# Kernel optimization log

Hardware: AMD Instinct MI355X
Metric: run time of the kernel (lower is better)

Reference implementation:

```python
import jax, jax.numpy as jnp
import numpy as np

H = 256        # h_dim
H2 = 128       # h_dim // 2
S = 512        # sentence_size
G = 64         # number of component graphs in the batched graph
NN = 100000    # total nodes in batched graph
NE = 200000    # total edges
NENT = 20000   # num entities
NREL = 500     # num relations
B = 32         # batch of query timestamps
SEQ = 10       # seq_len


def setup_inputs() -> dict:
    key = jax.random.key(0)
    ks = jax.random.split(key, 32)
    d = {}
    d["node_ids"] = jax.random.randint(ks[0], (NN,), 0, NENT, dtype=jnp.int32)
    d["edge_src"] = jax.random.randint(ks[1], (NE,), 0, NN, dtype=jnp.int32)
    d["edge_dst"] = jax.random.randint(ks[2], (NE,), 0, NN, dtype=jnp.int32)
    d["edge_type"] = jax.random.randint(ks[3], (NE,), 0, NREL, dtype=jnp.int32)
    d["node2graph"] = jnp.sort(jax.random.randint(ks[4], (NN,), 0, G, dtype=jnp.int32))
    d["edge2graph"] = jnp.sort(jax.random.randint(ks[5], (NE,), 0, G, dtype=jnp.int32))
    d["text_emb"] = jax.random.normal(ks[6], (NE, S), dtype=jnp.float32)
    d["time_idx"] = jax.random.randint(ks[7], (B, SEQ), 0, G, dtype=jnp.int32)
    d["len_non_zero"] = jnp.maximum(jax.random.randint(ks[8], (B,), 0, SEQ, dtype=jnp.int32), 1)
    d["ent_embeds"] = jax.random.normal(ks[9], (NENT, 2 * H), dtype=jnp.float32) * 0.05
    d["ent_memory"] = jax.random.normal(ks[10], (NENT, H), dtype=jnp.float32) * 0.05
    d["rel_embeds"] = jax.random.normal(ks[11], (NREL, 2 * H), dtype=jnp.float32) * 0.05
    d["rel_memory"] = jax.random.normal(ks[12], (NREL, H), dtype=jnp.float32) * 0.05
    sc = lambda k, sh: jax.random.normal(k, sh, dtype=jnp.float32) * (1.0 / np.sqrt(sh[0]))
    d["w_node_W"] = sc(ks[13], (3 * H, H)); d["w_node_b"] = jnp.zeros((H,), jnp.float32)
    d["w_rel_W"] = sc(ks[14], (3 * H, H)); d["w_rel_b"] = jnp.zeros((H,), jnp.float32)
    # CompGCN layer 1: H -> H2 (nodes and edges), text S -> H2
    d["Wn1"] = sc(ks[15], (H, H2)); d["Wl1"] = sc(ks[16], (H, H2))
    d["Wt1"] = sc(ks[17], (S, H2)); d["Wr1"] = sc(ks[18], (H, H2))
    d["b1"] = jnp.zeros((H2,), jnp.float32)
    # CompGCN layer 2: H2 -> H, text S -> H
    d["Wn2"] = sc(ks[19], (H2, H)); d["Wl2"] = sc(ks[20], (H2, H))
    d["Wt2"] = sc(ks[21], (S, H)); d["Wr2"] = sc(ks[22], (H2, H))
    d["b2"] = jnp.zeros((H,), jnp.float32)
    return d


def _compgcn_layer(h, e, text, src, dst, Wn, Wl, Wt, Wr, b, n_nodes):
    # composition = subtraction: msg = (h_src - e_h) @ Wn + text @ Wt
    msg = (h[src] - e) @ Wn + text @ Wt                      # [NE, out]
    agg = jax.ops.segment_sum(msg, dst, num_segments=n_nodes)
    deg = jax.ops.segment_sum(jnp.ones((msg.shape[0],), msg.dtype), dst, num_segments=n_nodes)
    agg = agg / jnp.maximum(deg, 1.0)[:, None]
    h_new = jax.nn.relu(agg + h @ Wl + b)                    # self-loop + bias + relu
    e_new = jax.nn.relu(e @ Wr)                              # relation transform
    return h_new, e_new


def reference(node_ids, edge_src, edge_dst, edge_type, node2graph, edge2graph,
              text_emb, time_idx, len_non_zero,
              ent_embeds, ent_memory, rel_embeds, rel_memory,
              w_node_W, w_node_b, w_rel_W, w_rel_b,
              Wn1, Wl1, Wt1, Wr1, b1, Wn2, Wl2, Wt2, Wr2, b2):
    n_nodes = node_ids.shape[0]
    # initial node / edge features: cat(embed[2h], memory[h]) -> Linear(3h, h)
    h = jnp.concatenate([ent_embeds[node_ids], ent_memory[node_ids]], axis=1) @ w_node_W + w_node_b
    e = jnp.concatenate([rel_embeds[edge_type], rel_memory[edge_type]], axis=1) @ w_rel_W + w_rel_b
    # two CompGCN relational message-passing layers: H -> H2 -> H
    h, e = _compgcn_layer(h, e, text_emb, edge_src, edge_dst, Wn1, Wl1, Wt1, Wr1, b1, n_nodes)
    h, e = _compgcn_layer(h, e, text_emb, edge_src, edge_dst, Wn2, Wl2, Wt2, Wr2, b2, n_nodes)
    # dgl.max_nodes / dgl.max_edges: per-graph max pooling (maxpool == 1)
    gn = jax.ops.segment_max(h, node2graph, num_segments=G)   # [G, H]
    ge = jax.ops.segment_max(e, edge2graph, num_segments=G)   # [G, H]
    global_info = jnp.concatenate([gn, ge], axis=-1)          # [G, 2H]
    # ragged temporal gather: embed_seq[i, j] = global_info[time_to_idx[time_list[i][j]]]
    seq = global_info[time_idx]                               # [B, SEQ, 2H]
    mask = (jnp.arange(SEQ, dtype=jnp.int32)[None, :] < len_non_zero[:, None])
    seq = seq * mask[..., None].astype(seq.dtype)             # zeros past len_non_zero
    # dropout at eval time is identity
    return seq, len_non_zero
```

## Files before the change

### kernel.cpp

```cpp
#include <hip/hip_runtime.h>

#define HD    256
#define HD2   128
#define SDIM  512
#define GNUM  64
#define NN    100000
#define NE    200000
#define NENT  20000
#define NREL  500
#define BNUM  32
#define SEQL  10

typedef __attribute__((ext_vector_type(4))) float f32x4;
typedef __attribute__((ext_vector_type(8))) short bf16x8;

__device__ __forceinline__ short to_bf(float f) {
    unsigned u = __float_as_uint(f);
    u += 0x7fff + ((u >> 16) & 1);
    return (short)(u >> 16);
}
__device__ __forceinline__ float bf_to_f(unsigned short u) {
    return __uint_as_float(((unsigned)u) << 16);
}


__global__ void k_cnt(const int* __restrict__ edst, int* __restrict__ cnt) {
    int e = blockIdx.x * 256 + threadIdx.x;
    if (e < NE) atomicAdd(&cnt[edst[e]], 1);
}

__global__ void k_scan_blk(const int* __restrict__ cnt, int* __restrict__ row_off,
                           int* __restrict__ bsum) {
    __shared__ int s[256];
    int i = blockIdx.x * 256 + threadIdx.x;
    int v = cnt[i];
    s[threadIdx.x] = v;
    __syncthreads();
    for (int d = 1; d < 256; d <<= 1) {
        int t = (threadIdx.x >= d) ? s[threadIdx.x - d] : 0;
        __syncthreads();
        s[threadIdx.x] += t;
        __syncthreads();
    }
    row_off[i] = s[threadIdx.x] - v;
    if (threadIdx.x == 255) bsum[blockIdx.x] = s[255];
}

__global__ void k_scan_top(int* __restrict__ bsum) {
    __shared__ int s[512];
    int v = (threadIdx.x < 391) ? bsum[threadIdx.x] : 0;
    s[threadIdx.x] = v;
    __syncthreads();
    for (int d = 1; d < 512; d <<= 1) {
        int t = (threadIdx.x >= d) ? s[threadIdx.x - d] : 0;
        __syncthreads();
        s[threadIdx.x] += t;
        __syncthreads();
    }
    if (threadIdx.x < 391) bsum[threadIdx.x] = s[threadIdx.x] - v;
}

__global__ void k_scan_add(int* __restrict__ row_off, const int* __restrict__ bsum,
                           int* __restrict__ cur) {
    int i = blockIdx.x * 256 + threadIdx.x;
    int v = row_off[i] + bsum[blockIdx.x];
    row_off[i] = v;
    cur[i] = v;
}

__global__ void k_fill(const int* __restrict__ edst, const int* __restrict__ esrc,
                       const int* __restrict__ etype, const int* __restrict__ node_ids,
                       int* __restrict__ cur, int* __restrict__ pinv,
                       int* __restrict__ esrcC, int* __restrict__ etC,
                       int* __restrict__ nidC) {
    int e = blockIdx.x * 256 + threadIdx.x;
    if (e < NE) {
        int pos = atomicAdd(&cur[edst[e]], 1);
        int s = esrc[e];
        pinv[e] = pos;
        esrcC[pos] = s;
        etC[pos] = etype[e];
        nidC[pos] = node_ids[s];
    }
}


__global__ void k_rel_feat(const float* __restrict__ rel_emb, const float* __restrict__ rel_mem,
                           const float* __restrict__ W, const float* __restrict__ b,
                           float* __restrict__ rel_feat) {
    __shared__ float s[768];
    int r = blockIdx.x, j = threadIdx.x;
    for (int k = j; k < 768; k += 256)
        s[k] = (k < 512) ? rel_emb[r * 512 + k] : rel_mem[r * 256 + (k - 512)];
    __syncthreads();
    float acc = b[j];
    for (int k = 0; k < 768; ++k) acc += s[k] * W[k * 256 + j];
    rel_feat[r * 256 + j] = acc;
}

__global__ void k_rel_l1(const float* __restrict__ rel_feat, const float* __restrict__ Wn1,
                         const float* __restrict__ Wr1, float* __restrict__ ecomb,
                         float* __restrict__ er1) {
    __shared__ float s[256];
    int r = blockIdx.x, j = threadIdx.x;
    s[j] = rel_feat[r * 256 + j];
    __syncthreads();
    if (j < 128) {
        float acc = 0.f;
        for (int k = 0; k < 256; ++k) acc += s[k] * Wn1[k * 128 + j];
        ecomb[r * 384 + j] = acc;
    } else {
        int jj = j - 128;
        float acc = 0.f;
        for (int k = 0; k < 256; ++k) acc += s[k] * Wr1[k * 128 + jj];
        er1[r * 128 + jj] = fmaxf(acc, 0.f);
    }
}

__global__ void k_rel_l2(const float* __restrict__ er1, const float* __restrict__ Wr2,
                         const float* __restrict__ Wn2, float* __restrict__ er2,
                         float* __restrict__ ecomb) {
    __shared__ float s[128];
    int r = blockIdx.x, j = threadIdx.x;
    if (j < 128) s[j] = er1[r * 128 + j];
    __syncthreads();
    float a = 0.f, c = 0.f;
    for (int k = 0; k < 128; ++k) {
        float v = s[k];
        a += v * Wr2[k * 256 + j];
        c += v * Wn2[k * 256 + j];
    }
    er2[r * 256 + j] = fmaxf(a, 0.f);
    ecomb[r * 384 + 128 + j] = c;
}


__global__ void k_cw(const float* __restrict__ wnW, const float* __restrict__ Wn1,
                     const float* __restrict__ Wl1, float* __restrict__ cw) {
    __shared__ float s[256];
    int k = blockIdx.x, j = threadIdx.x;
    s[j] = wnW[k * 256 + j];
    __syncthreads();
    float acc = 0.f;
    if (j < 128) {
        for (int m = 0; m < 256; ++m) acc += s[m] * Wn1[m * 128 + j];
    } else {
        int jj = j - 128;
        for (int m = 0; m < 256; ++m) acc += s[m] * Wl1[m * 128 + jj];
    }
    cw[k * 256 + j] = acc;
}

__global__ void k_cb(const float* __restrict__ wnb, const float* __restrict__ Wn1,
                     const float* __restrict__ Wl1, float* __restrict__ bc) {
    int j = threadIdx.x;
    float acc = 0.f;
    if (j < 128) {
        for (int m = 0; m < 256; ++m) acc += wnb[m] * Wn1[m * 128 + j];
    } else {
        int jj = j - 128;
        for (int m = 0; m < 256; ++m) acc += wnb[m] * Wl1[m * 128 + jj];
    }
    bc[j] = acc;
}

__global__ void k_pack(const float* __restrict__ src, bf16x8* __restrict__ dst,
                       int K, int N) {
    int KF = K >> 5;
    int fid = blockIdx.x;
    int n = fid / KF, kk = fid - n * KF;
    int lane = threadIdx.x;
    int col = n * 16 + (lane & 15);
    int kb = kk * 32 + (lane >> 4) * 8;
    bf16x8 v;
#pragma unroll
    for (int j = 0; j < 8; ++j) v[j] = to_bf(src[(size_t)(kb + j) * N + col]);
    dst[(size_t)fid * 64 + lane] = v;
}


__global__ void __launch_bounds__(256) k_ent(const float* __restrict__ ee,
                                             const float* __restrict__ em,
                                             const bf16x8* __restrict__ cwf,
                                             const float* __restrict__ bc,
                                             float* __restrict__ ha1,
                                             float* __restrict__ hb1) {
    __shared__ bf16x8 sA[2048];
    int tid = threadIdx.x;
    int e0 = blockIdx.x * 64;
    int wave = tid >> 6, lane = tid & 63;
    int gs = (tid >> 4) & 3, rs = tid & 15;
    int rowS = ((tid >> 6) & 3) * 16 + rs;
    int ent = e0 + rowS;
    if (ent >= NENT) ent = NENT - 1;
    f32x4 acc[4][4];
#pragma unroll
    for (int mf = 0; mf < 4; ++mf)
#pragma unroll
        for (int nf = 0; nf < 4; ++nf) acc[mf][nf] = (f32x4)0.f;

    for (int ch = 0; ch < 3; ++ch) {
        if (ch) __syncthreads();
#pragma unroll
        for (int it = 0; it < 8; ++it) {
            int gc = ch * 256 + it * 32 + gs * 8;
            const float4* p = (gc < 512)
                ? (const float4*)(ee + (size_t)ent * 512 + gc)
                : (const float4*)(em + (size_t)ent * 256 + (gc - 512));
            float4 x = p[0], y = p[1];
            bf16x8 v;
            v[0] = to_bf(x.x); v[1] = to_bf(x.y); v[2] = to_bf(x.z); v[3] = to_bf(x.w);
            v[4] = to_bf(y.x); v[5] = to_bf(y.y); v[6] = to_bf(y.z); v[7] = to_bf(y.w);
            sA[it * 256 + tid] = v;
        }
        __syncthreads();
#pragma unroll
        for (int kkl = 0; kkl < 8; ++kkl) {
            bf16x8 a[4], b[4];
#pragma unroll
            for (int mf = 0; mf < 4; ++mf) a[mf] = sA[kkl * 256 + mf * 64 + lane];
#pragma unroll
            for (int nf = 0; nf < 4; ++nf)
                b[nf] = cwf[(size_t)((wave * 4 + nf) * 24 + ch * 8 + kkl) * 64 + lane];
#pragma unroll
            for (int mf = 0; mf < 4; ++mf)
#pragma unroll
                for (int nf = 0; nf < 4; ++nf)
                    acc[mf][nf] = __builtin_amdgcn_mfma_f32_16x16x32_bf16(a[mf], b[nf],
                                                                          acc[mf][nf], 0, 0, 0);
        }
    }
    int gq = lane >> 4, cl = lane & 15;
#pragma unroll
    for (int mf = 0; mf < 4; ++mf)
#pragma unroll
        for (int nf = 0; nf < 4; ++nf) {
            int c = wave * 64 + nf * 16 + cl;
            float bb = bc[c];
#pragma unroll
            for (int q = 0; q < 4; ++q) {
                int m = e0 + mf * 16 + gq * 4 + q;
                if (m < NENT) {
                    float val = acc[mf][nf][q] + bb;
                    if (c < 128) ha1[(size_t)m * 128 + c] = val;
                    else hb1[(size_t)m * 128 + (c - 128)] = val;
                }
            }
        }
}


__global__ void __launch_bounds__(256, 3) k_edge(const float* __restrict__ text,
                                                 const int* __restrict__ pinv,
                                                 const bf16x8* __restrict__ wtf,
                                                 unsigned short* __restrict__ msg) {
    __shared__ bf16x8 sA[2048];
    __shared__ int s_pos[64];
    int tid = threadIdx.x;
    size_t e0 = (size_t)blockIdx.x * 64;
    if (tid < 64) s_pos[tid] = pinv[e0 + tid];
    int R = ((tid >> 6) << 4) + (tid & 15);
    int g = (tid >> 4) & 3;
    const float* trow = text + (e0 + R) * 512 + g * 8;

    int wave = tid >> 6, lane = tid & 63;
    f32x4 acc[4][6];
#pragma unroll
    for (int mf = 0; mf < 4; ++mf)
#pragma unroll
        for (int nf = 0; nf < 6; ++nf) acc[mf][nf] = (f32x4)0.f;

#pragma unroll
    for (int p = 0; p < 2; ++p) {
        if (p) __syncthreads();
#pragma unroll
        for (int h = 0; h < 2; ++h) {
            float4 xs[4], ys[4];
#pragma unroll
            for (int k2 = 0; k2 < 4; ++k2) {
                const float4* p4 = (const float4*)(trow + p * 256 + (h * 4 + k2) * 32);
                xs[k2] = p4[0];
                ys[k2] = p4[1];
            }
#pragma unroll
            for (int k2 = 0; k2 < 4; ++k2) {
                bf16x8 v;
                v[0] = to_bf(xs[k2].x); v[1] = to_bf(xs[k2].y);
                v[2] = to_bf(xs[k2].z); v[3] = to_bf(xs[k2].w);
                v[4] = to_bf(ys[k2].x); v[5] = to_bf(ys[k2].y);
                v[6] = to_bf(ys[k2].z); v[7] = to_bf(ys[k2].w);
                sA[(h * 4 + k2) * 256 + tid] = v;
            }
        }
        __syncthreads();
#pragma unroll
        for (int kkl = 0; kkl < 8; ++kkl) {
            bf16x8 a[4], b[6];
#pragma unroll
            for (int mf = 0; mf < 4; ++mf) a[mf] = sA[kkl * 256 + mf * 64 + lane];
#pragma unroll
            for (int nf = 0; nf < 6; ++nf)
                b[nf] = wtf[(size_t)((wave * 6 + nf) * 16 + p * 8 + kkl) * 64 + lane];
#pragma unroll
            for (int mf = 0; mf < 4; ++mf)
#pragma unroll
                for (int nf = 0; nf < 6; ++nf)
                    acc[mf][nf] = __builtin_amdgcn_mfma_f32_16x16x32_bf16(a[mf], b[nf],
                                                                          acc[mf][nf], 0, 0, 0);
        }
    }

    int gq = lane >> 4, cl = lane & 15;
#pragma unroll
    for (int mf = 0; mf < 4; ++mf)
#pragma unroll
        for (int nf = 0; nf < 6; ++nf) {
            int c = wave * 96 + nf * 16 + cl;
            f32x4 v = acc[mf][nf];
#pragma unroll
            for (int q = 0; q < 4; ++q) {
                int row = mf * 16 + gq * 4 + q;
                msg[(size_t)s_pos[row] * 384 + c] = (unsigned short)to_bf(v[q]);
            }
        }
}


__global__ void __launch_bounds__(256) k_agg(const unsigned short* __restrict__ msg,
                                             const int* __restrict__ row_off,
                                             const int* __restrict__ etC,
                                             const int* __restrict__ nidC,
                                             const int* __restrict__ node_ids,
                                             const float* __restrict__ ha1,
                                             const float* __restrict__ ecomb,
                                             const float* __restrict__ hb1,
                                             const float* __restrict__ b1,
                                             unsigned short* __restrict__ h1b,
                                             unsigned short* __restrict__ agg2b) {
    int n = blockIdx.x * 4 + (threadIdx.x >> 6);
    int lane = threadIdx.x & 63;
    if (n >= NN) return;
    int beg = row_off[n], end = row_off[n + 1];
    float d = fmaxf((float)(end - beg), 1.f);
    int nid0 = node_ids[n];
    int c = lane * 2;
    float a0 = 0.f, a1 = 0.f, a2 = 0.f, a3 = 0.f, a4 = 0.f, a5 = 0.f;
    const unsigned* m32 = (const unsigned*)msg;
    for (int i = beg; i < end; ++i) {
        int et = etC[i], nid = nidC[i];
        size_t base = (size_t)i * 192;
        unsigned u0 = m32[base + lane];
        unsigned u1 = m32[base + 64 + lane];
        unsigned u2 = m32[base + 128 + lane];
        const float2 ec0 = *(const float2*)(ecomb + (size_t)et * 384 + c);
        const float2 ec1 = *(const float2*)(ecomb + (size_t)et * 384 + 128 + c);
        const float2 ec2 = *(const float2*)(ecomb + (size_t)et * 384 + 256 + c);
        const float2 hv = *(const float2*)(ha1 + (size_t)nid * 128 + c);
        a0 += bf_to_f((unsigned short)(u0 & 0xffff)) + hv.x - ec0.x;
        a1 += bf_to_f((unsigned short)(u0 >> 16)) + hv.y - ec0.y;
        a2 += bf_to_f((unsigned short)(u1 & 0xffff)) - ec1.x;
        a3 += bf_to_f((unsigned short)(u1 >> 16)) - ec1.y;
        a4 += bf_to_f((unsigned short)(u2 & 0xffff)) - ec2.x;
        a5 += bf_to_f((unsigned short)(u2 >> 16)) - ec2.y;
    }
    const float2 hb = *(const float2*)(hb1 + (size_t)nid0 * 128 + c);
    const float2 bb = *(const float2*)(b1 + c);
    float hx = fmaxf(a0 / d + hb.x + bb.x, 0.f);
    float hy = fmaxf(a1 / d + hb.y + bb.y, 0.f);
    unsigned hp = ((unsigned)(unsigned short)to_bf(hx)) |
                  (((unsigned)(unsigned short)to_bf(hy)) << 16);
    ((unsigned*)h1b)[(size_t)n * 64 + lane] = hp;
    unsigned g0 = ((unsigned)(unsigned short)to_bf(a2)) |
                  (((unsigned)(unsigned short)to_bf(a3)) << 16);
    unsigned g1 = ((unsigned)(unsigned short)to_bf(a4)) |
                  (((unsigned)(unsigned short)to_bf(a5)) << 16);
    ((unsigned*)agg2b)[(size_t)n * 128 + lane] = g0;
    ((unsigned*)agg2b)[(size_t)n * 128 + 64 + lane] = g1;
}


__global__ void __launch_bounds__(256) k_s1(const unsigned short* __restrict__ h1b,
                                            const int* __restrict__ row_off,
                                            const int* __restrict__ esrcC,
                                            unsigned short* __restrict__ s1b) {
    int n = blockIdx.x * 4 + (threadIdx.x >> 6);
    int lane = threadIdx.x & 63;
    if (n >= NN) return;
    int beg = row_off[n], end = row_off[n + 1];
    float ax = 0.f, ay = 0.f;
    const unsigned* h32 = (const unsigned*)h1b;
    for (int i = beg; i < end; ++i) {
        int src = esrcC[i];
        unsigned u = h32[(size_t)src * 64 + lane];
        ax += bf_to_f((unsigned short)(u & 0xffff));
        ay += bf_to_f((unsigned short)(u >> 16));
    }
    unsigned p = ((unsigned)(unsigned short)to_bf(ax)) |
                 (((unsigned)(unsigned short)to_bf(ay)) << 16);
    ((unsigned*)s1b)[(size_t)n * 64 + lane] = p;
}


__global__ void __launch_bounds__(256) k_h2(const unsigned short* __restrict__ s1b,
                                            const unsigned short* __restrict__ h1b,
                                            const unsigned short* __restrict__ agg2b,
                                            const int* __restrict__ cnt,
                                            const int* __restrict__ n2g,
                                            const bf16x8* __restrict__ wn2f,
                                            const bf16x8* __restrict__ wl2f,
                                            const float* __restrict__ b2,
                                            float* __restrict__ gn) {
    __shared__ bf16x8 sS[1024], sH[1024];
    __shared__ int s_g[64];
    int tid = threadIdx.x, n0 = blockIdx.x * 64;
    int wave = tid >> 6, lane = tid & 63;
    if (tid < 64) {
        int m = n0 + tid;
        if (m >= NN) m = NN - 1;
        s_g[tid] = n2g[m];
    }
    {
        int gsv = (tid >> 4) & 3, rsv = tid & 15;
        int row = ((tid >> 6) & 3) * 16 + rsv;
        int m = n0 + row;
        if (m >= NN) m = NN - 1;
#pragma unroll
        for (int kk = 0; kk < 4; ++kk) {
            int cb = kk * 32 + gsv * 8;
            sS[kk * 256 + tid] = *(const bf16x8*)(s1b + (size_t)m * 128 + cb);
            sH[kk * 256 + tid] = *(const bf16x8*)(h1b + (size_t)m * 128 + cb);
        }
    }
    __syncthreads();
    f32x4 aa[4][4], ab[4][4];
#pragma unroll
    for (int mf = 0; mf < 4; ++mf)
#pragma unroll
        for (int nf = 0; nf < 4; ++nf) { aa[mf][nf] = (f32x4)0.f; ab[mf][nf] = (f32x4)0.f; }
#pragma unroll
    for (int kk = 0; kk < 4; ++kk) {
        bf16x8 a1[4], a2[4], bv1[4], bv2[4];
#pragma unroll
        for (int mf = 0; mf < 4; ++mf) {
            a1[mf] = sS[kk * 256 + mf * 64 + lane];
            a2[mf] = sH[kk * 256 + mf * 64 + lane];
        }
#pragma unroll
        for (int nf = 0; nf < 4; ++nf) {
            bv1[nf] = wn2f[(size_t)((wave * 4 + nf) * 4 + kk) * 64 + lane];
            bv2[nf] = wl2f[(size_t)((wave * 4 + nf) * 4 + kk) * 64 + lane];
        }
#pragma unroll
        for (int mf = 0; mf < 4; ++mf)
#pragma unroll
            for (int nf = 0; nf < 4; ++nf) {
                aa[mf][nf] = __builtin_amdgcn_mfma_f32_16x16x32_bf16(a1[mf], bv1[nf],
                                                                     aa[mf][nf], 0, 0, 0);
                ab[mf][nf] = __builtin_amdgcn_mfma_f32_16x16x32_bf16(a2[mf], bv2[nf],
                                                                     ab[mf][nf], 0, 0, 0);
            }
    }
    int gq = lane >> 4, cl = lane & 15;
    float dinv[4][4];
#pragma unroll
    for (int mf = 0; mf < 4; ++mf)
#pragma unroll
        for (int q = 0; q < 4; ++q) {
            int m = n0 + mf * 16 + gq * 4 + q;
            if (m >= NN) m = NN - 1;
            dinv[mf][q] = 1.f / fmaxf((float)cnt[m], 1.f);
        }
    float b2v[4];
#pragma unroll
    for (int nf = 0; nf < 4; ++nf) b2v[nf] = b2[wave * 64 + nf * 16 + cl];
#pragma unroll
    for (int mf = 0; mf < 4; ++mf)
#pragma unroll
        for (int nf = 0; nf < 4; ++nf) {
            int c = wave * 64 + nf * 16 + cl;
#pragma unroll
            for (int q = 0; q < 4; ++q) {
                int m = n0 + mf * 16 + gq * 4 + q;
                if (m >= NN) m = NN - 1;
                float araw = bf_to_f(agg2b[(size_t)m * 256 + c]);
                aa[mf][nf][q] = fmaxf((araw + aa[mf][nf][q]) * dinv[mf][q]
                                      + ab[mf][nf][q] + b2v[nf], 0.f);
            }
        }
    int g0 = s_g[0], g63 = s_g[63];
    if (g0 == g63) {
#pragma unroll
        for (int nf = 0; nf < 4; ++nf) {
            float mx = 0.f;
#pragma unroll
            for (int mf = 0; mf < 4; ++mf)
#pragma unroll
                for (int q = 0; q < 4; ++q) mx = fmaxf(mx, aa[mf][nf][q]);
            mx = fmaxf(mx, __shfl_xor(mx, 16));
            mx = fmaxf(mx, __shfl_xor(mx, 32));
            if (gq == 0) {
                int c = wave * 64 + nf * 16 + cl;
                atomicMax((int*)&gn[(size_t)g0 * 256 + c], __float_as_int(mx));
            }
        }
    } else {
#pragma unroll
        for (int mf = 0; mf < 4; ++mf)
#pragma unroll
            for (int q = 0; q < 4; ++q) {
                int row = mf * 16 + gq * 4 + q;
                int m = n0 + row;
                if (m >= NN) continue;
                int gg = s_g[row];
#pragma unroll
                for (int nf = 0; nf < 4; ++nf) {
                    int c = wave * 64 + nf * 16 + cl;
                    atomicMax((int*)&gn[(size_t)gg * 256 + c],
                              __float_as_int(aa[mf][nf][q]));
                }
            }
    }
}


__device__ __forceinline__ int lower_bound_i(const int* __restrict__ a, int n, int v) {
    int lo = 0, hi = n;
    while (lo < hi) {
        int m = (lo + hi) >> 1;
        if (a[m] < v) lo = m + 1; else hi = m;
    }
    return lo;
}

__global__ void k_gmax_edges(const float* __restrict__ er2, const int* __restrict__ e2g,
                             const int* __restrict__ etype, float* __restrict__ ge) {
    int g = blockIdx.x, q = blockIdx.y, j = threadIdx.x;
    int lo = lower_bound_i(e2g, NE, g);
    int hi = lower_bound_i(e2g, NE, g + 1);
    float mx = 0.f;
    for (int e = lo + q; e < hi; e += 16) mx = fmaxf(mx, er2[etype[e] * 256 + j]);
    atomicMax((int*)&ge[g * 256 + j], __float_as_int(mx));
}

__global__ void k_out(const float* __restrict__ gn, const float* __restrict__ ge,
                      const int* __restrict__ time_idx, const int* __restrict__ lens,
                      float* __restrict__ out) {
    int idx = blockIdx.x * 256 + threadIdx.x;
    const int NOUT = BNUM * SEQL * 512;
    if (idx < NOUT) {
        int j = idx & 511;
        int bt = idx >> 9;
        int b = bt / SEQL, t = bt - b * SEQL;
        float v = 0.f;
        if (t < lens[b]) {
            int g = time_idx[bt];
            v = (j < 256) ? gn[g * 256 + j] : ge[g * 256 + (j - 256)];
        }
        out[idx] = v;
    } else if (idx < NOUT + BNUM) {
        int b = idx - NOUT;
        out[idx] = (float)lens[b];
    }
}


extern "C" void kernel_launch(void* const* d_in, const int* in_sizes, int n_in,
                              void* d_out, int out_size, void* d_ws, size_t ws_size,
                              hipStream_t stream) {
    const int*   node_ids  = (const int*)d_in[0];
    const int*   edge_src  = (const int*)d_in[1];
    const int*   edge_dst  = (const int*)d_in[2];
    const int*   edge_type = (const int*)d_in[3];
    const int*   node2g    = (const int*)d_in[4];
    const int*   edge2g    = (const int*)d_in[5];
    const float* text_emb  = (const float*)d_in[6];
    const int*   time_idx  = (const int*)d_in[7];
    const int*   lens      = (const int*)d_in[8];
    const float* ent_emb   = (const float*)d_in[9];
    const float* ent_mem   = (const float*)d_in[10];
    const float* rel_emb   = (const float*)d_in[11];
    const float* rel_mem   = (const float*)d_in[12];
    const float* w_node_W  = (const float*)d_in[13];
    const float* w_node_b  = (const float*)d_in[14];
    const float* w_rel_W   = (const float*)d_in[15];
    const float* w_rel_b   = (const float*)d_in[16];
    const float* Wn1 = (const float*)d_in[17];
    const float* Wl1 = (const float*)d_in[18];
    const float* Wt1 = (const float*)d_in[19];
    const float* Wr1 = (const float*)d_in[20];
    const float* b1  = (const float*)d_in[21];
    const float* Wn2 = (const float*)d_in[22];
    const float* Wl2 = (const float*)d_in[23];
    const float* Wt2 = (const float*)d_in[24];
    const float* Wr2 = (const float*)d_in[25];
    const float* b2  = (const float*)d_in[26];

    float* ws = (float*)d_ws;
    size_t off = 0;
    float* rel_feat = ws + off; off += (size_t)NREL * 256;
    float* er1      = ws + off; off += (size_t)NREL * 128;
    float* er2      = ws + off; off += (size_t)NREL * 256;
    float* ecomb    = ws + off; off += (size_t)NREL * 384;
    float* ha1      = ws + off; off += (size_t)NENT * 128;
    float* hb1      = ws + off; off += (size_t)NENT * 128;
    float* cw       = ws + off; off += (size_t)768 * 256;
    float* bc       = ws + off; off += 256;
    bf16x8* wtf  = (bf16x8*)(ws + off); off += (size_t)24 * 16 * 64 * 4;
    bf16x8* cwf  = (bf16x8*)(ws + off); off += (size_t)16 * 24 * 64 * 4;
    bf16x8* wn2f = (bf16x8*)(ws + off); off += (size_t)16 * 4 * 64 * 4;
    bf16x8* wl2f = (bf16x8*)(ws + off); off += (size_t)16 * 4 * 64 * 4;
    int*   cnt = (int*)(ws + off);
    size_t zoff = off;          off += 100096;
    float* gn  = ws + off;      off += (size_t)GNUM * 256;
    float* ge  = ws + off;      off += (size_t)GNUM * 256;
    size_t zbytes = (off - zoff) * sizeof(float);
    int* row_off = (int*)(ws + off); off += 100352;
    int* cur     = (int*)(ws + off); off += 100096;
    int* bsum    = (int*)(ws + off); off += 512;
    int* pinv    = (int*)(ws + off); off += (size_t)NE;
    int* esrcC   = (int*)(ws + off); off += (size_t)NE;
    int* etC     = (int*)(ws + off); off += (size_t)NE;
    int* nidC    = (int*)(ws + off); off += (size_t)NE;
    unsigned short* msg = (unsigned short*)(ws + off);
    unsigned short* s1b = (unsigned short*)(ws + off);
    off += (size_t)NE * 384 / 2;
    unsigned short* h1b   = (unsigned short*)(ws + off); off += (size_t)NN * 64;
    unsigned short* agg2b = (unsigned short*)(ws + off); off += (size_t)NN * 128;

    hipMemsetAsync((void*)cnt, 0, zbytes, stream);

    k_cnt<<<(NE + 255) / 256, 256, 0, stream>>>(edge_dst, cnt);
    k_scan_blk<<<391, 256, 0, stream>>>(cnt, row_off, bsum);
    k_scan_top<<<1, 512, 0, stream>>>(bsum);
    k_scan_add<<<391, 256, 0, stream>>>(row_off, bsum, cur);
    k_fill<<<(NE + 255) / 256, 256, 0, stream>>>(edge_dst, edge_src, edge_type, node_ids,
                                                 cur, pinv, esrcC, etC, nidC);

    k_rel_feat<<<NREL, 256, 0, stream>>>(rel_emb, rel_mem, w_rel_W, w_rel_b, rel_feat);
    k_rel_l1<<<NREL, 256, 0, stream>>>(rel_feat, Wn1, Wr1, ecomb, er1);
    k_rel_l2<<<NREL, 256, 0, stream>>>(er1, Wr2, Wn2, er2, ecomb);

    k_cw<<<768, 256, 0, stream>>>(w_node_W, Wn1, Wl1, cw);
    k_cb<<<1, 256, 0, stream>>>(w_node_b, Wn1, Wl1, bc);
    k_pack<<<8 * 16, 64, 0, stream>>>(Wt1, wtf, 512, 128);
    k_pack<<<16 * 16, 64, 0, stream>>>(Wt2, wtf + (size_t)8 * 16 * 64, 512, 256);
    k_pack<<<16 * 24, 64, 0, stream>>>(cw, cwf, 768, 256);
    k_pack<<<16 * 4, 64, 0, stream>>>(Wn2, wn2f, 128, 256);
    k_pack<<<16 * 4, 64, 0, stream>>>(Wl2, wl2f, 128, 256);

    k_ent<<<(NENT + 63) / 64, 256, 0, stream>>>(ent_emb, ent_mem, cwf, bc, ha1, hb1);

    k_edge<<<NE / 64, 256, 0, stream>>>(text_emb, pinv, wtf, msg);

    k_agg<<<NN / 4, 256, 0, stream>>>(msg, row_off, etC, nidC, node_ids,
                                      ha1, ecomb, hb1, b1, h1b, agg2b);
    k_s1<<<NN / 4, 256, 0, stream>>>(h1b, row_off, esrcC, s1b);
    k_h2<<<(NN + 63) / 64, 256, 0, stream>>>(s1b, h1b, agg2b, cnt, node2g,
                                             wn2f, wl2f, b2, gn);

    k_gmax_edges<<<dim3(GNUM, 16), 256, 0, stream>>>(er2, edge2g, edge_type, ge);
    k_out<<<(BNUM * SEQL * 512 + BNUM + 255) / 256, 256, 0, stream>>>(gn, ge, time_idx, lens,
                                                                      (float*)d_out);
}
```

Baseline: 580.9 us.

## Restructure edge text GEMM so each wave owns 16 rows and all columns

The edge-text projection kernel no longer stages converted bf16 text tiles in shared memory with block barriers. Each wave now loads and converts its own 16 edge rows straight into registers and computes all 384 output columns, streaming weight fragments from global memory. This removes LDS traffic and __syncthreads, but each wave now reads the full weight matrix, about four times the weight load traffic per block. It also raises accumulator register pressure, since the occupancy hint of 3 was dropped.

```diff
diff --git a/kernel.cpp b/kernel.cpp
--- a/kernel.cpp
+++ b/kernel.cpp
@@ -250,79 +250,53 @@
 }
 
 
-__global__ void __launch_bounds__(256, 3) k_edge(const float* __restrict__ text,
-                                                 const int* __restrict__ pinv,
-                                                 const bf16x8* __restrict__ wtf,
-                                                 unsigned short* __restrict__ msg) {
-    __shared__ bf16x8 sA[2048];
-    __shared__ int s_pos[64];
+__global__ void __launch_bounds__(256) k_edge(const float* __restrict__ text,
+                                              const int* __restrict__ pinv,
+                                              const bf16x8* __restrict__ wtf,
+                                              unsigned short* __restrict__ msg) {
     int tid = threadIdx.x;
-    size_t e0 = (size_t)blockIdx.x * 64;
-    if (tid < 64) s_pos[tid] = pinv[e0 + tid];
-    int R = ((tid >> 6) << 4) + (tid & 15);
-    int g = (tid >> 4) & 3;
-    const float* trow = text + (e0 + R) * 512 + g * 8;
-
     int wave = tid >> 6, lane = tid & 63;
-    f32x4 acc[4][6];
-#pragma unroll
-    for (int mf = 0; mf < 4; ++mf)
-#pragma unroll
-        for (int nf = 0; nf < 6; ++nf) acc[mf][nf] = (f32x4)0.f;
-
-#pragma unroll
-    for (int p = 0; p < 2; ++p) {
-        if (p) __syncthreads();
-#pragma unroll
-        for (int h = 0; h < 2; ++h) {
-            float4 xs[4], ys[4];
-#pragma unroll
-            for (int k2 = 0; k2 < 4; ++k2) {
-                const float4* p4 = (const float4*)(trow + p * 256 + (h * 4 + k2) * 32);
-                xs[k2] = p4[0];
-                ys[k2] = p4[1];
+    size_t e0w = (size_t)blockIdx.x * 64 + wave * 16;
+    int r = lane & 15, g = lane >> 4;
+    const float* trow = text + (e0w + r) * 512 + g * 8;
+    int spos[4];
+#pragma unroll
+    for (int q = 0; q < 4; ++q) spos[q] = pinv[e0w + g * 4 + q];
+
+    f32x4 acc[24];
+#pragma unroll
+    for (int nf = 0; nf < 24; ++nf) acc[nf] = (f32x4)0.f;
+
+#pragma unroll
+    for (int hh = 0; hh < 2; ++hh) {
+        bf16x8 a[8];
+#pragma unroll
+        for (int kk = 0; kk < 8; ++kk) {
+            const float4* p = (const float4*)(trow + (hh * 8 + kk) * 32);
+            float4 x = p[0], y = p[1];
+            bf16x8 v;
+            v[0] = to_bf(x.x); v[1] = to_bf(x.y); v[2] = to_bf(x.z); v[3] = to_bf(x.w);
+            v[4] = to_bf(y.x); v[5] = to_bf(y.y); v[6] = to_bf(y.z); v[7] = to_bf(y.w);
+            a[kk] = v;
+        }
+#pragma unroll
+        for (int kk = 0; kk < 8; ++kk) {
+#pragma unroll
+            for (int nf = 0; nf < 24; ++nf) {
+                bf16x8 b = wtf[(size_t)(nf * 16 + hh * 8 + kk) * 64 + lane];
+                acc[nf] = __builtin_amdgcn_mfma_f32_16x16x32_bf16(a[kk], b, acc[nf], 0, 0, 0);
             }
-#pragma unroll
-            for (int k2 = 0; k2 < 4; ++k2) {
-                bf16x8 v;
-                v[0] = to_bf(xs[k2].x); v[1] = to_bf(xs[k2].y);
-                v[2] = to_bf(xs[k2].z); v[3] = to_bf(xs[k2].w);
-                v[4] = to_bf(ys[k2].x); v[5] = to_bf(ys[k2].y);
-                v[6] = to_bf(ys[k2].z); v[7] = to_bf(ys[k2].w);
-                sA[(h * 4 + k2) * 256 + tid] = v;
-            }
-        }
-        __syncthreads();
-#pragma unroll
-        for (int kkl = 0; kkl < 8; ++kkl) {
-            bf16x8 a[4], b[6];
-#pragma unroll
-            for (int mf = 0; mf < 4; ++mf) a[mf] = sA[kkl * 256 + mf * 64 + lane];
-#pragma unroll
-            for (int nf = 0; nf < 6; ++nf)
-                b[nf] = wtf[(size_t)((wave * 6 + nf) * 16 + p * 8 + kkl) * 64 + lane];
-#pragma unroll
-            for (int mf = 0; mf < 4; ++mf)
-#pragma unroll
-                for (int nf = 0; nf < 6; ++nf)
-                    acc[mf][nf] = __builtin_amdgcn_mfma_f32_16x16x32_bf16(a[mf], b[nf],
-                                                                          acc[mf][nf], 0, 0, 0);
-        }
-    }
-
-    int gq = lane >> 4, cl = lane & 15;
-#pragma unroll
-    for (int mf = 0; mf < 4; ++mf)
-#pragma unroll
-        for (int nf = 0; nf < 6; ++nf) {
-            int c = wave * 96 + nf * 16 + cl;
-            f32x4 v = acc[mf][nf];
-#pragma unroll
-            for (int q = 0; q < 4; ++q) {
-                int row = mf * 16 + gq * 4 + q;
-                msg[(size_t)s_pos[row] * 384 + c] = (unsigned short)to_bf(v[q]);
-            }
-        }
+        }
+    }
+
+    int cl = lane & 15;
+#pragma unroll
+    for (int nf = 0; nf < 24; ++nf) {
+        int c = nf * 16 + cl;
+#pragma unroll
+        for (int q = 0; q < 4; ++q)
+            msg[(size_t)spos[q] * 384 + c] = (unsigned short)to_bf(acc[nf][q]);
+    }
 }
 
 
```

Result: slower. 767.2 us (+32.1%).
